# Optimization experiments

Measured on AMD Instinct MI355X. Metric: run time of the kernel, lower is better.

The kernel has to match this reference:

```python
import jax, jax.numpy as jnp
import numpy as np

D_MODEL = 512
N_HEADS = 8
D_HEAD = 64
INIT_RANGE = 0.02
IGNORE = -1.0e6
SINK = -1000.0


def setup_inputs() -> dict:
    key = jax.random.key(0)
    ks = jax.random.split(key, 7)
    bs, ts = 2, 128
    x = jax.random.normal(ks[0], (bs, ts, D_MODEL), dtype=jnp.float32)
    W_K1 = INIT_RANGE * jax.random.normal(ks[1], (N_HEADS, D_MODEL, D_HEAD), dtype=jnp.float32)
    W_K2 = INIT_RANGE * jax.random.normal(ks[2], (N_HEADS, D_MODEL, D_HEAD), dtype=jnp.float32)
    W_Q = INIT_RANGE * jax.random.normal(ks[3], (N_HEADS, D_MODEL, D_HEAD), dtype=jnp.float32)
    W_V12 = INIT_RANGE * jax.random.normal(ks[4], (N_HEADS, 2 * D_MODEL, D_HEAD), dtype=jnp.float32)
    W_O = INIT_RANGE * jax.random.normal(ks[5], (N_HEADS, D_HEAD, D_MODEL), dtype=jnp.float32)
    b_K1 = jnp.zeros((N_HEADS, D_HEAD), dtype=jnp.float32)
    b_K2 = jnp.zeros((N_HEADS, D_HEAD), dtype=jnp.float32)
    b_Q = jnp.zeros((N_HEADS, D_HEAD), dtype=jnp.float32)
    b_V12 = jnp.zeros((N_HEADS, D_HEAD), dtype=jnp.float32)
    b_O = jnp.zeros((D_MODEL,), dtype=jnp.float32)
    return {"x": x, "W_K1": W_K1, "W_K2": W_K2, "W_Q": W_Q, "W_V12": W_V12,
            "W_O": W_O, "b_K1": b_K1, "b_K2": b_K2, "b_Q": b_Q, "b_V12": b_V12, "b_O": b_O}


def _trittention(x, W_K1, W_K2, W_Q, W_V12, W_O, b_K1, b_K2, b_Q, b_V12, b_O):
    bs, ts, d = x.shape
    nh, dh = W_K1.shape[0], W_K1.shape[2]
    k1 = jnp.einsum('ndh,bpd->bpnh', W_K1, x) + b_K1
    k2 = jnp.einsum('ndh,bpd->bpnh', W_K2, x) + b_K2
    q = jnp.einsum('ndh,bpd->bpnh', W_Q, x) + b_Q
    # pairwise values: v[b,p,s] = cat(x[b,p], x[b,s]) @ W_V12 + b_V12
    Wa, Wb = W_V12[:, :d, :], W_V12[:, d:, :]
    va = jnp.einsum('ndh,bpd->bpnh', Wa, x)   # [b, ts, n, h]
    vb = jnp.einsum('ndh,bsd->bsnh', Wb, x)
    v = va[:, :, None] + vb[:, None] + b_V12  # [b, p, s, n, h]
    # cubic scores [b, n, s, t, q]
    scores = jnp.einsum('bsnh,btnh,bqnh->bnstq', k1, k2, q)
    ia = jnp.arange(ts)[:, None, None]  # s axis (k1)
    ib = jnp.arange(ts)[None, :, None]  # t axis (k2)
    ic = jnp.arange(ts)[None, None, :]  # q axis
    # attn_eq=False, order_attn=True
    mask = (ia >= ic) | (ib >= ic) | (ia >= ib)
    scores = jnp.where(mask, IGNORE, scores)
    # b n s t q -> b n q (s t), scale, append sink column
    scores = jnp.transpose(scores, (0, 1, 4, 2, 3)).reshape(bs, nh, ts, ts * ts) / dh
    sink = jnp.full((bs, nh, ts, 1), SINK, dtype=scores.dtype)
    attn = jax.nn.softmax(jnp.concatenate([scores, sink], axis=-1), axis=-1)
    # b p s n h -> b n h (p s), append zero value column
    vf = jnp.transpose(v, (0, 3, 4, 1, 2)).reshape(bs, nh, dh, ts * ts)
    vf = jnp.concatenate([vf, jnp.zeros((bs, nh, dh, 1), dtype=vf.dtype)], axis=-1)
    z = jnp.einsum('bnql,bnhl->bqnh', attn, vf)
    out = jnp.einsum('bpnh,nhd->bpd', z, W_O) + b_O
    return out


def reference(x, W_K1, W_K2, W_Q, W_V12, W_O, b_K1, b_K2, b_Q, b_V12, b_O):
    return _trittention(x, W_K1, W_K2, W_Q, W_V12, W_O, b_K1, b_K2, b_Q, b_V12, b_O)
```

## Files before the change

kernel.cpp:

```cpp
#include <hip/hip_runtime.h>

#define BS 2
#define TS 128
#define DM 512
#define NH 8
#define DH 64
#define BN (BS*NH)

typedef __attribute__((ext_vector_type(8))) short short8;
typedef __attribute__((ext_vector_type(4))) float floatx4;

#define SEG (BN*TS*DH)
#define OFS_Q    0
#define OFS_VA   SEG
#define OFS_VB   (2*SEG)
#define OFS_K1B  (3*SEG)
#define OFS_K2B  (3*SEG + SEG/2)

__device__ __forceinline__ unsigned short f2bf(float x) {
  unsigned u = __float_as_uint(x);
  u += 0x7fff + ((u >> 16) & 1);
  return (unsigned short)(u >> 16);
}
__device__ __forceinline__ float bf2f(short v) {
  return __uint_as_float(((unsigned)(unsigned short)v) << 16);
}

__global__ __launch_bounds__(256) void proj_kernel(
    const float* __restrict__ x,   const float* __restrict__ Wk1,
    const float* __restrict__ Wk2, const float* __restrict__ Wq,
    const float* __restrict__ Wv12,const float* __restrict__ bk1,
    const float* __restrict__ bk2, const float* __restrict__ bq,
    const float* __restrict__ bo,  float* __restrict__ out,
    float* __restrict__ ws)
{
  int t = blockIdx.x;
  int rt = t & 3; t >>= 2;
  int n  = t & 7; t >>= 3;
  int proj = t;
  int tid = threadIdx.x;
  int wv = tid >> 6, ln = tid & 63, q4 = ln >> 4, l15 = ln & 15;

  for (int i = blockIdx.x*256 + tid; i < BS*TS*DM; i += 160*256)
    out[i] = bo[i & (DM-1)];

  const float* W;
  switch (proj) {
    case 0:  W = Wk1 + n*DM*DH;  break;
    case 1:  W = Wk2 + n*DM*DH;  break;
    case 2:  W = Wq  + n*DM*DH;  break;
    case 3:  W = Wv12 + n*2*DM*DH;  break;
    default: W = Wv12 + n*2*DM*DH + DM*DH;  break;
  }

  __shared__ __align__(16) short xb [64][520];
  __shared__ __align__(16) short wbt[64][520];

  for (int v = tid; v < 8192; v += 256) {
    int r = v >> 7, c = (v & 127) * 4;
    float4 xv = *(const float4*)&x[(size_t)(rt*64 + r)*DM + c];
    uint2 pk;
    pk.x = (unsigned)f2bf(xv.x) | ((unsigned)f2bf(xv.y) << 16);
    pk.y = (unsigned)f2bf(xv.z) | ((unsigned)f2bf(xv.w) << 16);
    *(uint2*)&xb[r][c] = pk;
  }
  {
    int nn = ln, kc8 = wv;
    for (int p = 0; p < 16; ++p) {
      int k0 = p*32 + kc8*8;
      unsigned short tmp[8];
      #pragma unroll
      for (int jj = 0; jj < 8; ++jj) tmp[jj] = f2bf(W[(k0 + jj)*DH + nn]);
      uint4 pk;
      pk.x = tmp[0] | ((unsigned)tmp[1] << 16);
      pk.y = tmp[2] | ((unsigned)tmp[3] << 16);
      pk.z = tmp[4] | ((unsigned)tmp[5] << 16);
      pk.w = tmp[6] | ((unsigned)tmp[7] << 16);
      *(uint4*)&wbt[nn][k0] = pk;
    }
  }
  __syncthreads();

  short8 afr[16];
  #pragma unroll
  for (int kc = 0; kc < 16; ++kc)
    afr[kc] = *(const short8*)&xb[wv*16 + l15][kc*32 + q4*8];

  floatx4 acc[4];
  #pragma unroll
  for (int nt = 0; nt < 4; ++nt) {
    floatx4 c = (floatx4){0.f,0.f,0.f,0.f};
    #pragma unroll
    for (int kc = 0; kc < 16; ++kc) {
      short8 bfr = *(const short8*)&wbt[nt*16 + l15][kc*32 + q4*8];
      c = __builtin_amdgcn_mfma_f32_16x16x32_bf16(afr[kc], bfr, c, 0,0,0);
    }
    acc[nt] = c;
  }

  #pragma unroll
  for (int nt = 0; nt < 4; ++nt) {
    int col = nt*16 + l15;
    float bias = 0.f;
    if (proj == 0) bias = bk1[n*DH + col];
    else if (proj == 1) bias = bk2[n*DH + col];
    else if (proj == 2) bias = bq[n*DH + col];
    #pragma unroll
    for (int r = 0; r < 4; ++r) {
      int row = rt*64 + wv*16 + q4*4 + r;
      int b = row >> 7, s = row & 127;
      size_t o = (size_t)((b*NH + n)*TS + s)*DH + col;
      float v = acc[nt][r] + bias;
      switch (proj) {
        case 0: ((unsigned short*)(ws + OFS_K1B))[o] = f2bf(v); break;
        case 1: ((unsigned short*)(ws + OFS_K2B))[o] = f2bf(v); break;
        case 2: ws[OFS_Q + o] = v; break;
        case 3: ws[OFS_VA + o] = v; break;
        default: ws[OFS_VB + o] = v; break;
      }
    }
  }
}

__global__ __launch_bounds__(256) void attn_kernel(
    const float* __restrict__ ws, const float* __restrict__ bv12,
    const float* __restrict__ Wo, float* __restrict__ out)
{
  int q  = blockIdx.x & 127;
  int bn = blockIdx.x >> 7;
  int tid = threadIdx.x;
  int wv = tid >> 6, ln = tid & 63, q4 = ln >> 4, l15 = ln & 15;
  int b = bn >> 3, n = bn & 7;

  if (q < 2) return;

  const unsigned short* k1g = (const unsigned short*)(ws + OFS_K1B) + (size_t)bn*TS*DH;
  const unsigned short* k2g = (const unsigned short*)(ws + OFS_K2B) + (size_t)bn*TS*DH;
  const float* qg  = ws + OFS_Q  + ((size_t)bn*TS + q)*DH;
  const float* vag = ws + OFS_VA + (size_t)bn*TS*DH;
  const float* vbg = ws + OFS_VB + (size_t)bn*TS*DH;

  __shared__ __align__(16) short Bh[128][72];
  __shared__ float Rs[128];
  __shared__ float Cp[4][128];
  __shared__ float Cs[128];
  __shared__ float zpart[4][64];
  __shared__ float dpart[4];
  __shared__ float zs[64];

  ((float*)Cp)[tid] = 0.f; ((float*)Cp)[tid + 256] = 0.f;

  int T = (q + 15) >> 4;
  for (int i = tid; i < T*128; i += 256) {
    int r = i >> 3, c = (i & 7) * 8;
    short8 kv = *(const short8*)&k2g[r*DH + c];
    float4 q0 = *(const float4*)&qg[c];
    float4 q1 = *(const float4*)&qg[c + 4];
    unsigned short o8[8];
    o8[0] = f2bf(bf2f(kv[0]) * q0.x); o8[1] = f2bf(bf2f(kv[1]) * q0.y);
    o8[2] = f2bf(bf2f(kv[2]) * q0.z); o8[3] = f2bf(bf2f(kv[3]) * q0.w);
    o8[4] = f2bf(bf2f(kv[4]) * q1.x); o8[5] = f2bf(bf2f(kv[5]) * q1.y);
    o8[6] = f2bf(bf2f(kv[6]) * q1.z); o8[7] = f2bf(bf2f(kv[7]) * q1.w);
    uint4 pk;
    pk.x = o8[0] | ((unsigned)o8[1] << 16);
    pk.y = o8[2] | ((unsigned)o8[3] << 16);
    pk.z = o8[4] | ((unsigned)o8[5] << 16);
    pk.w = o8[6] | ((unsigned)o8[7] << 16);
    *(uint4*)&Bh[r][c] = pk;
  }

  short8 afr[2][2];
  #pragma unroll
  for (int si2 = 0; si2 < 2; ++si2) {
    int m = (wv + 4*si2)*16 + l15;
    afr[si2][0] = *(const short8*)&k1g[m*DH + q4*8];
    afr[si2][1] = *(const short8*)&k1g[m*DH + q4*8 + 32];
  }
  __syncthreads();

  float rsum[2][4] = {{0.f,0.f,0.f,0.f},{0.f,0.f,0.f,0.f}};
  for (int tt = wv; tt < T; ++tt) {
    int tg = tt*16 + l15;
    short8 b0 = *(const short8*)&Bh[tg][q4*8];
    short8 b1 = *(const short8*)&Bh[tg][q4*8 + 32];
    float csum = 0.f;
    #pragma unroll
    for (int si2 = 0; si2 < 2; ++si2) {
      int si = wv + 4*si2;
      if (si > tt || 16*si >= q - 1) continue;
      floatx4 c = (floatx4){0.f,0.f,0.f,0.f};
      c = __builtin_amdgcn_mfma_f32_16x16x32_bf16(afr[si2][0], b0, c, 0,0,0);
      c = __builtin_amdgcn_mfma_f32_16x16x32_bf16(afr[si2][1], b1, c, 0,0,0);
      #pragma unroll
      for (int rg = 0; rg < 4; ++rg) {
        int s = si*16 + q4*4 + rg;
        float e = (s < tg && tg < q) ? __expf(c[rg] * 0.015625f) : 0.f;
        rsum[si2][rg] += e;
        csum += e;
      }
    }
    csum += __shfl_xor(csum, 16, 64);
    csum += __shfl_xor(csum, 32, 64);
    if (q4 == 0) Cp[wv][tg] = csum;
  }
  #pragma unroll
  for (int si2 = 0; si2 < 2; ++si2)
    #pragma unroll
    for (int rg = 0; rg < 4; ++rg) {
      float v = rsum[si2][rg];
      v += __shfl_xor(v, 1, 64); v += __shfl_xor(v, 2, 64);
      v += __shfl_xor(v, 4, 64); v += __shfl_xor(v, 8, 64);
      if (l15 == 0) Rs[(wv + 4*si2)*16 + q4*4 + rg] = v;
    }
  __syncthreads();

  if (tid < 128) Cs[tid] = Cp[0][tid] + Cp[1][tid] + Cp[2][tid] + Cp[3][tid];
  __syncthreads();

  int g = wv, h = ln;
  float acc = 0.f, dp = 0.f;
  int imax = (q + 3) >> 2;
  for (int i = 0; i < imax; ++i) {
    int s = g + 4*i;
    float rv = Rs[s], cv = Cs[s];
    acc = fmaf(rv, vag[s*DH + h], acc);
    acc = fmaf(cv, vbg[s*DH + h], acc);
    dp += rv;
  }
  zpart[g][h] = acc;
  if (ln == 0) dpart[g] = dp;
  __syncthreads();

  if (tid < 64) {
    float D = dpart[0] + dpart[1] + dpart[2] + dpart[3];
    zs[tid] = (zpart[0][tid] + zpart[1][tid] + zpart[2][tid] + zpart[3][tid]) / D
              + bv12[n*DH + tid];
  }
  __syncthreads();

  const float* WoN = Wo + (size_t)n*DH*DM;
  float* orow = out + (size_t)(b*TS + q)*DM;
  float a0 = 0.f, a1 = 0.f;
  #pragma unroll 8
  for (int h2 = 0; h2 < DH; ++h2) {
    float zv = zs[h2];
    a0 = fmaf(zv, WoN[h2*DM + tid],       a0);
    a1 = fmaf(zv, WoN[h2*DM + tid + 256], a1);
  }
  atomicAdd(&orow[tid],       a0);
  atomicAdd(&orow[tid + 256], a1);
}

extern "C" void kernel_launch(void* const* d_in, const int* in_sizes, int n_in,
                              void* d_out, int out_size, void* d_ws, size_t ws_size,
                              hipStream_t stream)
{
  const float* x    = (const float*)d_in[0];
  const float* Wk1  = (const float*)d_in[1];
  const float* Wk2  = (const float*)d_in[2];
  const float* Wq   = (const float*)d_in[3];
  const float* Wv12 = (const float*)d_in[4];
  const float* Wo   = (const float*)d_in[5];
  const float* bk1  = (const float*)d_in[6];
  const float* bk2  = (const float*)d_in[7];
  const float* bq   = (const float*)d_in[8];
  const float* bv12 = (const float*)d_in[9];
  const float* bo   = (const float*)d_in[10];
  float* out = (float*)d_out;
  float* ws  = (float*)d_ws;

  proj_kernel<<<5*NH*4, 256, 0, stream>>>(x, Wk1, Wk2, Wq, Wv12,
                                          bk1, bk2, bq, bo, out, ws);
  attn_kernel<<<BN*TS, 256, 0, stream>>>(ws, bv12, Wo, out);
}
```

Measured before the change: 117.0 us.

## Split output projection into separate GEMM kernel instead of per-row atomics

The attention kernel now writes per-head z vectors to a workspace buffer instead of multiplying by W_O and atomically accumulating into the output. A new out_kernel does the W_O projection for four rows per block and adds the bias, so the output no longer needs a bias pre-fill or atomic adds. This removes 2048 blocks each reading a 128KB slice of W_O and doing contended atomics, at the cost of an extra kernel launch and a global round-trip for z.

```diff
diff --git a/kernel.cpp b/kernel.cpp
--- a/kernel.cpp
+++ b/kernel.cpp
@@ -16,6 +16,7 @@
 #define OFS_VB   (2*SEG)
 #define OFS_K1B  (3*SEG)
 #define OFS_K2B  (3*SEG + SEG/2)
+#define OFS_Z    (4*SEG)
 
 __device__ __forceinline__ unsigned short f2bf(float x) {
   unsigned u = __float_as_uint(x);
@@ -31,7 +32,6 @@
     const float* __restrict__ Wk2, const float* __restrict__ Wq,
     const float* __restrict__ Wv12,const float* __restrict__ bk1,
     const float* __restrict__ bk2, const float* __restrict__ bq,
-    const float* __restrict__ bo,  float* __restrict__ out,
     float* __restrict__ ws)
 {
   int t = blockIdx.x;
@@ -40,9 +40,6 @@
   int proj = t;
   int tid = threadIdx.x;
   int wv = tid >> 6, ln = tid & 63, q4 = ln >> 4, l15 = ln & 15;
-
-  for (int i = blockIdx.x*256 + tid; i < BS*TS*DM; i += 160*256)
-    out[i] = bo[i & (DM-1)];
 
   const float* W;
   switch (proj) {
@@ -124,7 +121,7 @@
 
 __global__ __launch_bounds__(256) void attn_kernel(
     const float* __restrict__ ws, const float* __restrict__ bv12,
-    const float* __restrict__ Wo, float* __restrict__ out)
+    float* __restrict__ zb)
 {
   int q  = blockIdx.x & 127;
   int bn = blockIdx.x >> 7;
@@ -132,7 +129,10 @@
   int wv = tid >> 6, ln = tid & 63, q4 = ln >> 4, l15 = ln & 15;
   int b = bn >> 3, n = bn & 7;
 
-  if (q < 2) return;
+  if (q < 2) {
+    if (tid < 64) zb[(size_t)(b*TS + q)*DM + n*DH + tid] = 0.f;
+    return;
+  }
 
   const unsigned short* k1g = (const unsigned short*)(ws + OFS_K1B) + (size_t)bn*TS*DH;
   const unsigned short* k2g = (const unsigned short*)(ws + OFS_K2B) + (size_t)bn*TS*DH;
@@ -146,7 +146,6 @@
   __shared__ float Cs[128];
   __shared__ float zpart[4][64];
   __shared__ float dpart[4];
-  __shared__ float zs[64];
 
   ((float*)Cp)[tid] = 0.f; ((float*)Cp)[tid + 256] = 0.f;
 
@@ -233,22 +232,46 @@
 
   if (tid < 64) {
     float D = dpart[0] + dpart[1] + dpart[2] + dpart[3];
-    zs[tid] = (zpart[0][tid] + zpart[1][tid] + zpart[2][tid] + zpart[3][tid]) / D
-              + bv12[n*DH + tid];
-  }
-  __syncthreads();
-
-  const float* WoN = Wo + (size_t)n*DH*DM;
-  float* orow = out + (size_t)(b*TS + q)*DM;
-  float a0 = 0.f, a1 = 0.f;
-  #pragma unroll 8
-  for (int h2 = 0; h2 < DH; ++h2) {
-    float zv = zs[h2];
-    a0 = fmaf(zv, WoN[h2*DM + tid],       a0);
-    a1 = fmaf(zv, WoN[h2*DM + tid + 256], a1);
-  }
-  atomicAdd(&orow[tid],       a0);
-  atomicAdd(&orow[tid + 256], a1);
+    float zv = (zpart[0][tid] + zpart[1][tid] + zpart[2][tid] + zpart[3][tid]) / D
+               + bv12[n*DH + tid];
+    zb[(size_t)(b*TS + q)*DM + n*DH + tid] = zv;
+  }
+}
+
+__global__ __launch_bounds__(256) void out_kernel(
+    const float* __restrict__ z, const float* __restrict__ Wo,
+    const float* __restrict__ bo, float* __restrict__ out)
+{
+  int rb = blockIdx.x;
+  int tid = threadIdx.x;
+
+  __shared__ __align__(16) float zt[4][DM];
+  for (int i = tid; i < 4*DM/4; i += 256) {
+    int r = i >> 7, c4 = (i & 127) * 4;
+    *(float4*)&zt[r][c4] = *(const float4*)&z[(size_t)(rb*4 + r)*DM + c4];
+  }
+  __syncthreads();
+
+  float acc0[4] = {0.f,0.f,0.f,0.f};
+  float acc1[4] = {0.f,0.f,0.f,0.f};
+  const float* wp = Wo + tid;
+  #pragma unroll 4
+  for (int k = 0; k < DM; ++k) {
+    float w0 = wp[(size_t)k*DM];
+    float w1 = wp[(size_t)k*DM + 256];
+    #pragma unroll
+    for (int r = 0; r < 4; ++r) {
+      acc0[r] = fmaf(zt[r][k], w0, acc0[r]);
+      acc1[r] = fmaf(zt[r][k], w1, acc1[r]);
+    }
+  }
+
+  float b0 = bo[tid], b1 = bo[tid + 256];
+  #pragma unroll
+  for (int r = 0; r < 4; ++r) {
+    out[(size_t)(rb*4 + r)*DM + tid]       = acc0[r] + b0;
+    out[(size_t)(rb*4 + r)*DM + tid + 256] = acc1[r] + b1;
+  }
 }
 
 extern "C" void kernel_launch(void* const* d_in, const int* in_sizes, int n_in,
@@ -270,6 +293,7 @@
   float* ws  = (float*)d_ws;
 
   proj_kernel<<<5*NH*4, 256, 0, stream>>>(x, Wk1, Wk2, Wq, Wv12,
-                                          bk1, bk2, bq, bo, out, ws);
-  attn_kernel<<<BN*TS, 256, 0, stream>>>(ws, bv12, Wo, out);
-}
+                                          bk1, bk2, bq, ws);
+  attn_kernel<<<BN*TS, 256, 0, stream>>>(ws, bv12, ws + OFS_Z);
+  out_kernel<<<64, 256, 0, stream>>>(ws + OFS_Z, Wo, bo, out);
+}
```

New measurement: 145.4 us. +24.3%, slower.
